# Optimization experiments

Hardware: AMD Instinct MI355X
Metric: run time of the kernel (lower is better)

Reference implementation:

```python
import jax, jax.numpy as jnp
import numpy as np

N_TOKEN = 256
C_PAIR = 128
C = 32
N_HEADS = 4
LN_EPS = 1e-5


def setup_inputs() -> dict:
    key = jax.random.key(0)
    ks = jax.random.split(key, 8)
    w = lambda k, shape: jax.random.normal(k, shape, dtype=jnp.float32) * 0.02
    return {
        "pair": jax.random.normal(ks[0], (N_TOKEN, N_TOKEN, C_PAIR), dtype=jnp.float32),
        "gamma": jnp.ones((C_PAIR,), dtype=jnp.float32),
        "beta": jnp.zeros((C_PAIR,), dtype=jnp.float32),
        "Wq": w(ks[1], (C_PAIR, C * N_HEADS)),
        "Wk": w(ks[2], (C_PAIR, C * N_HEADS)),
        "Wv": w(ks[3], (C_PAIR, C * N_HEADS)),
        "Wb": w(ks[4], (C_PAIR, N_HEADS)),
        "Wg": w(ks[5], (C_PAIR, C * N_HEADS)),
        "Wout": w(ks[6], (C * N_HEADS, C_PAIR)),
    }


def _layernorm(x, gamma, beta):
    mu = jnp.mean(x, axis=-1, keepdims=True)
    var = jnp.mean(jnp.square(x - mu), axis=-1, keepdims=True)
    return (x - mu) * jax.lax.rsqrt(var + LN_EPS) * gamma + beta


def reference(pair, gamma, beta, Wq, Wk, Wv, Wb, Wg, Wout):
    n = pair.shape[0]
    pn = _layernorm(pair, gamma, beta)  # [N, N, c_pair]
    q = (pn @ Wq).reshape(n, n, N_HEADS, C)  # [i, j, h, c]
    k = (pn @ Wk).reshape(n, n, N_HEADS, C)  # [i, k, h, c]
    v = (pn @ Wv).reshape(n, n, N_HEADS, C)
    b = pn @ Wb                               # [j, k, h] pairwise bias
    g = jax.nn.sigmoid(pn @ Wg).reshape(n, n, N_HEADS, C)
    # a^h_ijk = softmax_k( q_ij . k_ik / sqrt(c) + b_jk )
    logits = jnp.einsum("ijhc,ikhc->ijkh", q, k) / np.float32(np.sqrt(C))
    logits = logits + b[None, :, :, :]        # broadcast over i: bias indexed by (j, k)
    attn = jax.nn.softmax(logits, axis=2)     # softmax over k axis
    o = jnp.einsum("ijkh,ikhc->ijhc", attn, v) * g
    return o.reshape(n, n, N_HEADS * C) @ Wout  # [N, N, c_pair]
```

## Files before the change

### kernel.cpp

```cpp
#include <hip/hip_runtime.h>

#define N_TOK 256
#define CP    128
#define CHD   32
#define NH    4
#define NT    65536
#define NCOL  528

typedef short short8 __attribute__((ext_vector_type(8)));
typedef float f32x4  __attribute__((ext_vector_type(4)));

__device__ __forceinline__ short f2bf(float f) {
    unsigned u = __builtin_bit_cast(unsigned, f);
    u += 0x7fffu + ((u >> 16) & 1u);
    return (short)(u >> 16);
}
__device__ __forceinline__ float bf2f(short s) {
    unsigned u = ((unsigned)(unsigned short)s) << 16;
    return __builtin_bit_cast(float, u);
}

__global__ void pack_weights(const float* __restrict__ Wq, const float* __restrict__ Wk,
                             const float* __restrict__ Wv, const float* __restrict__ Wb,
                             const float* __restrict__ Wg, const float* __restrict__ Wout,
                             short* __restrict__ wcat, short* __restrict__ woutT) {
    int idx = blockIdx.x * 256 + threadIdx.x;
    if (idx < NCOL * CP) {
        int n = idx >> 7, k = idx & 127;
        float v = 0.f;
        if (n < 512) {
            const float* W = (n < 128) ? Wq : (n < 256) ? Wk : (n < 384) ? Wv : Wg;
            v = W[k * 128 + (n & 127)];
        } else if (n < 516) {
            v = Wb[k * 4 + (n - 512)];
        }
        wcat[n * CP + k] = f2bf(v);
    } else {
        int j = idx - NCOL * CP;
        if (j < 128 * 128) {
            int n = j >> 7, k = j & 127;
            woutT[n * 128 + k] = f2bf(Wout[k * 128 + n]);
        }
    }
}

__global__ __launch_bounds__(256)
void ln_proj(const float* __restrict__ pair, const float* __restrict__ gamma,
             const float* __restrict__ beta, const short* __restrict__ wcat,
             short* __restrict__ qt, short* __restrict__ kt,
             short* __restrict__ vt, short* __restrict__ gt,
             float* __restrict__ bt) {
    __shared__ short pn[64 * 136];
    const int tid = threadIdx.x;
    const int wv = tid >> 6, lane = tid & 63;
    const int quad = lane >> 4, l15 = lane & 15;
    const int r0 = blockIdx.x * 64;

    float ga0 = gamma[2 * lane], ga1 = gamma[2 * lane + 1];
    float be0 = beta[2 * lane],  be1 = beta[2 * lane + 1];

    #pragma unroll 4
    for (int rr = 0; rr < 16; ++rr) {
        int row = wv * 16 + rr;
        const float* src = pair + (size_t)(r0 + row) * CP + 2 * lane;
        float x0 = src[0], x1 = src[1];
        float s = x0 + x1;
        #pragma unroll
        for (int m = 32; m; m >>= 1) s += __shfl_xor(s, m);
        float mu = s * (1.f / 128.f);
        float d0 = x0 - mu, d1 = x1 - mu;
        float vs = d0 * d0 + d1 * d1;
        #pragma unroll
        for (int m = 32; m; m >>= 1) vs += __shfl_xor(vs, m);
        float rs = rsqrtf(vs * (1.f / 128.f) + 1e-5f);
        short y0 = f2bf(d0 * rs * ga0 + be0);
        short y1 = f2bf(d1 * rs * ga1 + be1);
        unsigned pk = ((unsigned)(unsigned short)y0) | (((unsigned)(unsigned short)y1) << 16);
        *(unsigned*)&pn[row * 136 + 2 * lane] = pk;
    }
    __syncthreads();

    short8 afrag[4];
    #pragma unroll
    for (int s = 0; s < 4; ++s)
        afrag[s] = *(const short8*)&pn[(wv * 16 + l15) * 136 + s * 32 + quad * 8];

    for (int ch = 0; ch < 33; ++ch) {
        int n = ch * 16 + l15;
        f32x4 acc = {0.f, 0.f, 0.f, 0.f};
        #pragma unroll
        for (int s = 0; s < 4; ++s) {
            short8 bfrag = *(const short8*)&wcat[(size_t)n * CP + s * 32 + quad * 8];
            acc = __builtin_amdgcn_mfma_f32_16x16x32_bf16(afrag[s], bfrag, acc, 0, 0, 0);
        }
        if (ch < 32) {
            int arr = n >> 7;
            int h = (n >> 5) & 3, c = n & 31;
            short* dst = (arr == 0) ? qt : (arr == 1) ? kt : (arr == 2) ? vt : gt;
            size_t base = (size_t)h * NT * CHD + c;
            #pragma unroll
            for (int r = 0; r < 4; ++r) {
                int gr = r0 + wv * 16 + quad * 4 + r;
                float val = acc[r];
                if (arr == 3) val = 1.f / (1.f + __expf(-val));
                dst[base + (size_t)gr * CHD] = f2bf(val);
            }
        } else if (l15 < 4) {
            int h = l15;
            #pragma unroll
            for (int r = 0; r < 4; ++r) {
                int gr = r0 + wv * 16 + quad * 4 + r;
                bt[h * NT + gr] = acc[r];
            }
        }
    }
}

__global__ __launch_bounds__(256)
void attn(const short* __restrict__ qt, const short* __restrict__ kt,
          const short* __restrict__ vt, const short* __restrict__ gt,
          const float* __restrict__ bt, short* __restrict__ og) {
    __shared__ short vT[32 * 264];
    __shared__ short pl[64 * 264];
    const int tid = threadIdx.x;
    const int h = blockIdx.x >> 8, i = blockIdx.x & 255;
    const int wv = tid >> 6, lane = tid & 63;
    const int quad = lane >> 4, l15 = lane & 15;

    const short* kbase = kt + ((size_t)h * NT + (size_t)i * 256) * CHD;
    const short* vbase = vt + ((size_t)h * NT + (size_t)i * 256) * CHD;
    const short* qbase = qt + ((size_t)h * NT + (size_t)i * 256) * CHD;
    const short* gbase = gt + ((size_t)h * NT + (size_t)i * 256) * CHD;
    const float* bbase = bt + (size_t)h * NT;

    for (int g = tid; g < 1024; g += 256) {
        int key = g >> 2, p = g & 3;
        short8 s = *(const short8*)(vbase + key * CHD + p * 8);
        #pragma unroll
        for (int cc = 0; cc < 8; ++cc)
            vT[(p * 8 + cc) * 264 + key] = s[cc];
    }
    __syncthreads();

    const float scale = 0.17677669529663687f;

    for (int jt = 0; jt < 4; ++jt) {
        int jbase = jt * 64 + wv * 16;
        short8 aq = *(const short8*)(qbase + (jbase + l15) * CHD + quad * 8);

        f32x4 sacc[16];
        #pragma unroll
        for (int t = 0; t < 16; ++t) {
            short8 bk = *(const short8*)(kbase + (t * 16 + l15) * CHD + quad * 8);
            f32x4 z = {0.f, 0.f, 0.f, 0.f};
            sacc[t] = __builtin_amdgcn_mfma_f32_16x16x32_bf16(aq, bk, z, 0, 0, 0);
        }
        #pragma unroll
        for (int t = 0; t < 16; ++t)
            #pragma unroll
            for (int r = 0; r < 4; ++r) {
                int j = jbase + quad * 4 + r;
                sacc[t][r] = sacc[t][r] * scale + bbase[(size_t)j * 256 + t * 16 + l15];
            }
        float mx[4] = {-1e30f, -1e30f, -1e30f, -1e30f}, sm[4] = {0.f, 0.f, 0.f, 0.f};
        #pragma unroll
        for (int t = 0; t < 16; ++t)
            #pragma unroll
            for (int r = 0; r < 4; ++r) mx[r] = fmaxf(mx[r], sacc[t][r]);
        #pragma unroll
        for (int m = 1; m < 16; m <<= 1)
            #pragma unroll
            for (int r = 0; r < 4; ++r) mx[r] = fmaxf(mx[r], __shfl_xor(mx[r], m, 16));
        #pragma unroll
        for (int t = 0; t < 16; ++t)
            #pragma unroll
            for (int r = 0; r < 4; ++r) {
                float e = __expf(sacc[t][r] - mx[r]);
                sacc[t][r] = e;
                sm[r] += e;
            }
        #pragma unroll
        for (int m = 1; m < 16; m <<= 1)
            #pragma unroll
            for (int r = 0; r < 4; ++r) sm[r] += __shfl_xor(sm[r], m, 16);
        float inv[4];
        #pragma unroll
        for (int r = 0; r < 4; ++r) inv[r] = 1.f / sm[r];
        #pragma unroll
        for (int t = 0; t < 16; ++t)
            #pragma unroll
            for (int r = 0; r < 4; ++r)
                pl[(wv * 16 + quad * 4 + r) * 264 + t * 16 + l15] = f2bf(sacc[t][r] * inv[r]);
        __syncthreads();
        f32x4 oacc[2];
        oacc[0] = f32x4{0.f, 0.f, 0.f, 0.f};
        oacc[1] = f32x4{0.f, 0.f, 0.f, 0.f};
        #pragma unroll
        for (int ks = 0; ks < 8; ++ks) {
            short8 ap = *(const short8*)&pl[(wv * 16 + l15) * 264 + ks * 32 + quad * 8];
            #pragma unroll
            for (int nt = 0; nt < 2; ++nt) {
                short8 bv = *(const short8*)&vT[(nt * 16 + l15) * 264 + ks * 32 + quad * 8];
                oacc[nt] = __builtin_amdgcn_mfma_f32_16x16x32_bf16(ap, bv, oacc[nt], 0, 0, 0);
            }
        }
        #pragma unroll
        for (int nt = 0; nt < 2; ++nt) {
            int c = nt * 16 + l15;
            #pragma unroll
            for (int r = 0; r < 4; ++r) {
                int j = jbase + quad * 4 + r;
                float gv = bf2f(gbase[(size_t)j * CHD + c]);
                float o = oacc[nt][r] * gv;
                og[((size_t)i * 256 + j) * CP + h * CHD + c] = f2bf(o);
            }
        }
        __syncthreads();
    }
}

__global__ __launch_bounds__(256)
void out_gemm(const short* __restrict__ og, const short* __restrict__ woutT,
              float* __restrict__ out) {
    __shared__ short al[64 * 136];
    const int tid = threadIdx.x;
    const int wv = tid >> 6, lane = tid & 63;
    const int quad = lane >> 4, l15 = lane & 15;
    const int r0 = blockIdx.x * 64;

    for (int g = tid; g < 1024; g += 256) {
        int row = g >> 4, p = g & 15;
        *(short8*)&al[row * 136 + p * 8] = *(const short8*)(og + (size_t)(r0 + row) * CP + p * 8);
    }
    __syncthreads();

    short8 af[4];
    #pragma unroll
    for (int s = 0; s < 4; ++s)
        af[s] = *(const short8*)&al[(wv * 16 + l15) * 136 + s * 32 + quad * 8];

    #pragma unroll
    for (int ch = 0; ch < 8; ++ch) {
        int n = ch * 16 + l15;
        f32x4 acc = {0.f, 0.f, 0.f, 0.f};
        #pragma unroll
        for (int s = 0; s < 4; ++s) {
            short8 bfrag = *(const short8*)&woutT[(size_t)n * 128 + s * 32 + quad * 8];
            acc = __builtin_amdgcn_mfma_f32_16x16x32_bf16(af[s], bfrag, acc, 0, 0, 0);
        }
        #pragma unroll
        for (int r = 0; r < 4; ++r)
            out[(size_t)(r0 + wv * 16 + quad * 4 + r) * CP + n] = acc[r];
    }
}

extern "C" void kernel_launch(void* const* d_in, const int* in_sizes, int n_in,
                              void* d_out, int out_size, void* d_ws, size_t ws_size,
                              hipStream_t stream) {
    (void)in_sizes; (void)n_in; (void)out_size; (void)ws_size;
    const float* pair  = (const float*)d_in[0];
    const float* gamma = (const float*)d_in[1];
    const float* beta  = (const float*)d_in[2];
    const float* Wq    = (const float*)d_in[3];
    const float* Wk    = (const float*)d_in[4];
    const float* Wv    = (const float*)d_in[5];
    const float* Wb    = (const float*)d_in[6];
    const float* Wg    = (const float*)d_in[7];
    const float* Wout  = (const float*)d_in[8];
    float* out = (float*)d_out;

    char* ws = (char*)d_ws;
    const size_t SZ_QKVG = (size_t)NH * NT * CHD * 2;
    short* wcat  = (short*)(ws);
    short* woutT = (short*)(ws + 135168);
    short* qt    = (short*)(ws + 167936);
    short* kt    = (short*)(ws + 167936 + SZ_QKVG);
    short* vt    = (short*)(ws + 167936 + 2 * SZ_QKVG);
    short* gt    = (short*)(ws + 167936 + 3 * SZ_QKVG);
    float* bt    = (float*)(ws + 167936 + 4 * SZ_QKVG);
    short* og    = (short*)(ws + 167936 + 4 * SZ_QKVG + (size_t)NH * NT * 4);

    hipLaunchKernelGGL(pack_weights, dim3(328), dim3(256), 0, stream,
                       Wq, Wk, Wv, Wb, Wg, Wout, wcat, woutT);
    hipLaunchKernelGGL(ln_proj, dim3(1024), dim3(256), 0, stream,
                       pair, gamma, beta, wcat, qt, kt, vt, gt, bt);
    hipLaunchKernelGGL(attn, dim3(1024), dim3(256), 0, stream,
                       qt, kt, vt, gt, bt, og);
    hipLaunchKernelGGL(out_gemm, dim3(1024), dim3(256), 0, stream,
                       og, woutT, out);
}
```

Before: 226.3 us.

## Vectorize LayerNorm, stage projection outputs through LDS, swizzle attention LDS, drop barriers

LayerNorm now uses float4 loads with single-pass sum and sum-of-squares reductions over 32-lane halves. The projection epilogue goes through an LDS staging buffer so q/k/v/g are written as 16-byte coalesced stores instead of scattered 2-byte stores. The attention kernel replaces padded LDS rows with XOR-swizzled layouts to avoid bank conflicts and removes the per-tile __syncthreads, since each wave only touches its own rows of pl. Launch bounds are raised to 4 blocks per CU. Dropping the barriers in ln_proj (after LN and around sbuf) relies on each wave reading only rows it wrote, and the single-pass variance is less numerically stable.

```diff
diff --git a/kernel.cpp b/kernel.cpp
--- a/kernel.cpp
+++ b/kernel.cpp
@@ -6,9 +6,12 @@
 #define NH    4
 #define NT    65536
 #define NCOL  528
+#define PNS   136
 
 typedef short short8 __attribute__((ext_vector_type(8)));
 typedef float f32x4  __attribute__((ext_vector_type(4)));
+typedef float float4v __attribute__((ext_vector_type(4)));
+typedef unsigned uint2v __attribute__((ext_vector_type(2)));
 
 __device__ __forceinline__ short f2bf(float f) {
     unsigned u = __builtin_bit_cast(unsigned, f);
@@ -44,75 +47,91 @@
     }
 }
 
-__global__ __launch_bounds__(256)
+__global__ __launch_bounds__(256, 4)
 void ln_proj(const float* __restrict__ pair, const float* __restrict__ gamma,
              const float* __restrict__ beta, const short* __restrict__ wcat,
              short* __restrict__ qt, short* __restrict__ kt,
              short* __restrict__ vt, short* __restrict__ gt,
              float* __restrict__ bt) {
-    __shared__ short pn[64 * 136];
+    __shared__ short pn[64 * PNS];
+    __shared__ short sbuf[64 * PNS];
     const int tid = threadIdx.x;
     const int wv = tid >> 6, lane = tid & 63;
     const int quad = lane >> 4, l15 = lane & 15;
     const int r0 = blockIdx.x * 64;
-
-    float ga0 = gamma[2 * lane], ga1 = gamma[2 * lane + 1];
-    float be0 = beta[2 * lane],  be1 = beta[2 * lane + 1];
+    const int c = lane & 31, half = lane >> 5;
+
+    float4v ga = *(const float4v*)&gamma[4 * c];
+    float4v be = *(const float4v*)&beta[4 * c];
 
     #pragma unroll 4
-    for (int rr = 0; rr < 16; ++rr) {
-        int row = wv * 16 + rr;
-        const float* src = pair + (size_t)(r0 + row) * CP + 2 * lane;
-        float x0 = src[0], x1 = src[1];
-        float s = x0 + x1;
-        #pragma unroll
-        for (int m = 32; m; m >>= 1) s += __shfl_xor(s, m);
+    for (int p = 0; p < 8; ++p) {
+        int row = wv * 16 + p * 2 + half;
+        float4v x = *(const float4v*)(pair + (size_t)(r0 + row) * CP + 4 * c);
+        float s  = (x[0] + x[1]) + (x[2] + x[3]);
+        float q2 = (x[0] * x[0] + x[1] * x[1]) + (x[2] * x[2] + x[3] * x[3]);
+        #pragma unroll
+        for (int m = 1; m < 32; m <<= 1) {
+            s  += __shfl_xor(s, m, 32);
+            q2 += __shfl_xor(q2, m, 32);
+        }
         float mu = s * (1.f / 128.f);
-        float d0 = x0 - mu, d1 = x1 - mu;
-        float vs = d0 * d0 + d1 * d1;
-        #pragma unroll
-        for (int m = 32; m; m >>= 1) vs += __shfl_xor(vs, m);
-        float rs = rsqrtf(vs * (1.f / 128.f) + 1e-5f);
-        short y0 = f2bf(d0 * rs * ga0 + be0);
-        short y1 = f2bf(d1 * rs * ga1 + be1);
-        unsigned pk = ((unsigned)(unsigned short)y0) | (((unsigned)(unsigned short)y1) << 16);
-        *(unsigned*)&pn[row * 136 + 2 * lane] = pk;
-    }
-    __syncthreads();
+        float var = q2 * (1.f / 128.f) - mu * mu;
+        float rs = rsqrtf(var + 1e-5f);
+        unsigned y0 = (unsigned)(unsigned short)f2bf((x[0] - mu) * rs * ga[0] + be[0]);
+        unsigned y1 = (unsigned)(unsigned short)f2bf((x[1] - mu) * rs * ga[1] + be[1]);
+        unsigned y2 = (unsigned)(unsigned short)f2bf((x[2] - mu) * rs * ga[2] + be[2]);
+        unsigned y3 = (unsigned)(unsigned short)f2bf((x[3] - mu) * rs * ga[3] + be[3]);
+        uint2v pk = {y0 | (y1 << 16), y2 | (y3 << 16)};
+        *(uint2v*)&pn[row * PNS + 4 * c] = pk;
+    }
 
     short8 afrag[4];
     #pragma unroll
     for (int s = 0; s < 4; ++s)
-        afrag[s] = *(const short8*)&pn[(wv * 16 + l15) * 136 + s * 32 + quad * 8];
-
-    for (int ch = 0; ch < 33; ++ch) {
-        int n = ch * 16 + l15;
-        f32x4 acc = {0.f, 0.f, 0.f, 0.f};
-        #pragma unroll
-        for (int s = 0; s < 4; ++s) {
-            short8 bfrag = *(const short8*)&wcat[(size_t)n * CP + s * 32 + quad * 8];
-            acc = __builtin_amdgcn_mfma_f32_16x16x32_bf16(afrag[s], bfrag, acc, 0, 0, 0);
-        }
-        if (ch < 32) {
-            int arr = n >> 7;
-            int h = (n >> 5) & 3, c = n & 31;
-            short* dst = (arr == 0) ? qt : (arr == 1) ? kt : (arr == 2) ? vt : gt;
-            size_t base = (size_t)h * NT * CHD + c;
-            #pragma unroll
-            for (int r = 0; r < 4; ++r) {
-                int gr = r0 + wv * 16 + quad * 4 + r;
-                float val = acc[r];
-                if (arr == 3) val = 1.f / (1.f + __expf(-val));
-                dst[base + (size_t)gr * CHD] = f2bf(val);
-            }
-        } else if (l15 < 4) {
-            int h = l15;
-            #pragma unroll
-            for (int r = 0; r < 4; ++r) {
-                int gr = r0 + wv * 16 + quad * 4 + r;
-                bt[h * NT + gr] = acc[r];
-            }
-        }
+        afrag[s] = *(const short8*)&pn[(wv * 16 + l15) * PNS + s * 32 + quad * 8];
+
+    for (int grp = 0; grp < 4; ++grp) {
+        f32x4 acc[8];
+        #pragma unroll
+        for (int c8 = 0; c8 < 8; ++c8) {
+            acc[c8] = f32x4{0.f, 0.f, 0.f, 0.f};
+            #pragma unroll
+            for (int s = 0; s < 4; ++s) {
+                short8 bfrag = *(const short8*)&wcat[(size_t)(grp * 128 + c8 * 16 + l15) * CP + s * 32 + quad * 8];
+                acc[c8] = __builtin_amdgcn_mfma_f32_16x16x32_bf16(afrag[s], bfrag, acc[c8], 0, 0, 0);
+            }
+        }
+        if (grp == 3) {
+            #pragma unroll
+            for (int c8 = 0; c8 < 8; ++c8)
+                #pragma unroll
+                for (int r = 0; r < 4; ++r)
+                    acc[c8][r] = 1.f / (1.f + __expf(-acc[c8][r]));
+        }
+        #pragma unroll
+        for (int c8 = 0; c8 < 8; ++c8)
+            #pragma unroll
+            for (int r = 0; r < 4; ++r)
+                sbuf[(wv * 16 + quad * 4 + r) * PNS + c8 * 16 + l15] = f2bf(acc[c8][r]);
+        int row = wv * 16 + (lane >> 2);
+        short* dst = (grp == 0) ? qt : (grp == 1) ? kt : (grp == 2) ? vt : gt;
+        #pragma unroll
+        for (int rep = 0; rep < 4; ++rep) {
+            short8 v8 = *(const short8*)&sbuf[row * PNS + rep * 32 + (lane & 3) * 8];
+            *(short8*)(dst + ((size_t)rep * NT + r0 + row) * CHD + (lane & 3) * 8) = v8;
+        }
+    }
+    f32x4 accb = f32x4{0.f, 0.f, 0.f, 0.f};
+    #pragma unroll
+    for (int s = 0; s < 4; ++s) {
+        short8 bfrag = *(const short8*)&wcat[(size_t)(512 + l15) * CP + s * 32 + quad * 8];
+        accb = __builtin_amdgcn_mfma_f32_16x16x32_bf16(afrag[s], bfrag, accb, 0, 0, 0);
+    }
+    if (l15 < 4) {
+        #pragma unroll
+        for (int r = 0; r < 4; ++r)
+            bt[l15 * NT + r0 + wv * 16 + quad * 4 + r] = accb[r];
     }
 }
 
@@ -120,8 +139,8 @@
 void attn(const short* __restrict__ qt, const short* __restrict__ kt,
           const short* __restrict__ vt, const short* __restrict__ gt,
           const float* __restrict__ bt, short* __restrict__ og) {
-    __shared__ short vT[32 * 264];
-    __shared__ short pl[64 * 264];
+    __shared__ short vT[32 * 256];
+    __shared__ short pl[64 * 256];
     const int tid = threadIdx.x;
     const int h = blockIdx.x >> 8, i = blockIdx.x & 255;
     const int wv = tid >> 6, lane = tid & 63;
@@ -135,10 +154,13 @@
 
     for (int g = tid; g < 1024; g += 256) {
         int key = g >> 2, p = g & 3;
-        short8 s = *(const short8*)(vbase + key * CHD + p * 8);
-        #pragma unroll
-        for (int cc = 0; cc < 8; ++cc)
-            vT[(p * 8 + cc) * 264 + key] = s[cc];
+        short8 s8 = *(const short8*)(vbase + key * CHD + p * 8);
+        #pragma unroll
+        for (int cc = 0; cc < 8; ++cc) {
+            int row = p * 8 + cc;
+            int phys = (key >> 3) ^ (row & 7);
+            vT[row * 256 + phys * 8 + (key & 7)] = s8[cc];
+        }
     }
     __syncthreads();
 
@@ -189,40 +211,41 @@
         #pragma unroll
         for (int t = 0; t < 16; ++t)
             #pragma unroll
-            for (int r = 0; r < 4; ++r)
-                pl[(wv * 16 + quad * 4 + r) * 264 + t * 16 + l15] = f2bf(sacc[t][r] * inv[r]);
-        __syncthreads();
+            for (int r = 0; r < 4; ++r) {
+                int prow = wv * 16 + quad * 4 + r;
+                int phys = (2 * t + (l15 >> 3)) ^ (prow & 7);
+                pl[prow * 256 + phys * 8 + (l15 & 7)] = f2bf(sacc[t][r] * inv[r]);
+            }
         f32x4 oacc[2];
         oacc[0] = f32x4{0.f, 0.f, 0.f, 0.f};
         oacc[1] = f32x4{0.f, 0.f, 0.f, 0.f};
         #pragma unroll
         for (int ks = 0; ks < 8; ++ks) {
-            short8 ap = *(const short8*)&pl[(wv * 16 + l15) * 264 + ks * 32 + quad * 8];
+            int physp = ((ks * 4 + quad) ^ (l15 & 7)) * 8;
+            short8 ap = *(const short8*)&pl[(wv * 16 + l15) * 256 + physp];
             #pragma unroll
             for (int nt = 0; nt < 2; ++nt) {
-                short8 bv = *(const short8*)&vT[(nt * 16 + l15) * 264 + ks * 32 + quad * 8];
+                short8 bv = *(const short8*)&vT[(nt * 16 + l15) * 256 + physp];
                 oacc[nt] = __builtin_amdgcn_mfma_f32_16x16x32_bf16(ap, bv, oacc[nt], 0, 0, 0);
             }
         }
         #pragma unroll
         for (int nt = 0; nt < 2; ++nt) {
-            int c = nt * 16 + l15;
+            int cc = nt * 16 + l15;
             #pragma unroll
             for (int r = 0; r < 4; ++r) {
                 int j = jbase + quad * 4 + r;
-                float gv = bf2f(gbase[(size_t)j * CHD + c]);
-                float o = oacc[nt][r] * gv;
-                og[((size_t)i * 256 + j) * CP + h * CHD + c] = f2bf(o);
-            }
-        }
-        __syncthreads();
-    }
-}
-
-__global__ __launch_bounds__(256)
+                float gv = bf2f(gbase[(size_t)j * CHD + cc]);
+                og[((size_t)i * 256 + j) * CP + h * CHD + cc] = f2bf(oacc[nt][r] * gv);
+            }
+        }
+    }
+}
+
+__global__ __launch_bounds__(256, 4)
 void out_gemm(const short* __restrict__ og, const short* __restrict__ woutT,
               float* __restrict__ out) {
-    __shared__ short al[64 * 136];
+    __shared__ short al[64 * PNS];
     const int tid = threadIdx.x;
     const int wv = tid >> 6, lane = tid & 63;
     const int quad = lane >> 4, l15 = lane & 15;
@@ -230,28 +253,30 @@
 
     for (int g = tid; g < 1024; g += 256) {
         int row = g >> 4, p = g & 15;
-        *(short8*)&al[row * 136 + p * 8] = *(const short8*)(og + (size_t)(r0 + row) * CP + p * 8);
+        *(short8*)&al[row * PNS + p * 8] = *(const short8*)(og + (size_t)(r0 + row) * CP + p * 8);
     }
     __syncthreads();
 
     short8 af[4];
     #pragma unroll
     for (int s = 0; s < 4; ++s)
-        af[s] = *(const short8*)&al[(wv * 16 + l15) * 136 + s * 32 + quad * 8];
-
+        af[s] = *(const short8*)&al[(wv * 16 + l15) * PNS + s * 32 + quad * 8];
+
+    f32x4 acc[8];
     #pragma unroll
     for (int ch = 0; ch < 8; ++ch) {
-        int n = ch * 16 + l15;
-        f32x4 acc = {0.f, 0.f, 0.f, 0.f};
+        acc[ch] = f32x4{0.f, 0.f, 0.f, 0.f};
         #pragma unroll
         for (int s = 0; s < 4; ++s) {
-            short8 bfrag = *(const short8*)&woutT[(size_t)n * 128 + s * 32 + quad * 8];
-            acc = __builtin_amdgcn_mfma_f32_16x16x32_bf16(af[s], bfrag, acc, 0, 0, 0);
-        }
+            short8 bfrag = *(const short8*)&woutT[(size_t)(ch * 16 + l15) * 128 + s * 32 + quad * 8];
+            acc[ch] = __builtin_amdgcn_mfma_f32_16x16x32_bf16(af[s], bfrag, acc[ch], 0, 0, 0);
+        }
+    }
+    #pragma unroll
+    for (int ch = 0; ch < 8; ++ch)
         #pragma unroll
         for (int r = 0; r < 4; ++r)
-            out[(size_t)(r0 + wv * 16 + quad * 4 + r) * CP + n] = acc[r];
-    }
+            out[(size_t)(r0 + wv * 16 + quad * 4 + r) * CP + ch * 16 + l15] = acc[ch][r];
 }
 
 extern "C" void kernel_launch(void* const* d_in, const int* in_sizes, int n_in,
```

Result: slower. 244.5 us (+8.0%).
